# Kernel optimization log

Measured on AMD Instinct MI355X. Metric: run time of the kernel, lower is better.

## Reference

```python
import jax, jax.numpy as jnp
import numpy as np

MODEL_DIM = 256
PAIR_IMPORTANCE_WEIGHT = 0.5
B, S, D = 4, 4096, MODEL_DIM


def setup_inputs() -> dict:
    key = jax.random.key(0)
    ks = jax.random.split(key, 6)
    return {
        "query": jax.random.normal(ks[0], (B, S, D), dtype=jnp.float32),
        "key": jax.random.normal(ks[1], (B, S, D), dtype=jnp.float32),
        "value": jax.random.normal(ks[2], (B, S, D), dtype=jnp.float32),
        "W_query": jax.random.normal(ks[3], (D, D), dtype=jnp.float32),
        "W_key": jax.random.normal(ks[4], (D, D), dtype=jnp.float32),
        "W_value": jax.random.normal(ks[5], (D, D), dtype=jnp.float32),
    }


def reference(query, key, value, W_query, W_key, W_value):
    # Projections: [B,S,D] @ [D,D]
    q = jnp.einsum('bsd,de->bse', query, W_query)
    k = jnp.einsum('bsd,de->bse', key, W_key)
    v = jnp.einsum('bsd,de->bse', value, W_value)
    scale = jnp.sqrt(jnp.asarray(MODEL_DIM, dtype=q.dtype))
    # Full [B,S,S] score matrix (global max forces materialization)
    scores = jnp.einsum('bqd,bkd->bqk', q, k) / scale
    s_len = scores.shape[1]
    diag_bias = jnp.eye(s_len, dtype=scores.dtype) * jnp.max(scores)
    scores = scores + PAIR_IMPORTANCE_WEIGHT * diag_bias  # broadcast over batch
    attention_weights = jax.nn.softmax(scores, axis=-1)
    output = jnp.einsum('bqk,bkd->bqd', attention_weights, v)
    return output, attention_weights
```

## Files before the change

kernel.cpp:

```cpp
#include <hip/hip_runtime.h>
#include <cstdint>
#include <cstddef>

#define BB 4
#define SS 4096
#define DD 256
#define SCORE_SCALE (1.0f/16.0f)
#define PIW 0.5f

typedef float          f32x4  __attribute__((ext_vector_type(4)));
typedef __bf16         bf16v8 __attribute__((ext_vector_type(8)));
typedef unsigned short u16v8  __attribute__((ext_vector_type(8)));
typedef unsigned short u16v4  __attribute__((ext_vector_type(4)));

__device__ __forceinline__ f32x4 mfma_bf16(u16v8 a, u16v8 b, f32x4 c) {
    return __builtin_amdgcn_mfma_f32_16x16x32_bf16(
        __builtin_bit_cast(bf16v8, a), __builtin_bit_cast(bf16v8, b), c, 0, 0, 0);
}

__device__ __forceinline__ unsigned short f2bf(float f) {
    unsigned u = __float_as_uint(f);
    u += 0x7FFFu + ((u >> 16) & 1u);
    return (unsigned short)(u >> 16);
}
__device__ __forceinline__ float bf2f(unsigned short h) {
    return __uint_as_float(((unsigned)h) << 16);
}
__device__ __forceinline__ unsigned fenc(float x) {
    unsigned u = __float_as_uint(x);
    return (u & 0x80000000u) ? ~u : (u | 0x80000000u);
}
__device__ __forceinline__ float fdec(unsigned e) {
    return __uint_as_float((e & 0x80000000u) ? (e ^ 0x80000000u) : ~e);
}

#define TM 128
#define TN 128
#define TK 16
#define PADW 132

__global__ __launch_bounds__(256) void proj_kernel(
    const float* __restrict__ query, const float* __restrict__ key_, const float* __restrict__ value,
    const float* __restrict__ Wq, const float* __restrict__ Wk, const float* __restrict__ Wv,
    unsigned short* __restrict__ qh, unsigned short* __restrict__ ql,
    unsigned short* __restrict__ kh, unsigned short* __restrict__ kl,
    unsigned short* __restrict__ vT, unsigned* __restrict__ gmax)
{
    const int z = blockIdx.z;
    const float* A = (z == 0) ? query : (z == 1) ? key_ : value;
    const float* W = (z == 0) ? Wq    : (z == 1) ? Wk   : Wv;
    if (z == 0 && blockIdx.x == 0 && blockIdx.y == 0 && threadIdx.x == 0)
        *gmax = 0x007FFFFFu;

    const int K = DD, N = DD;
    __shared__ float As[TK][PADW];
    __shared__ float Bs[TK][PADW];
    const int tid = threadIdx.x;
    const int tx = tid & 15, ty = tid >> 4;
    const int rowBase = blockIdx.y * TM;
    const int colBase = blockIdx.x * TN;

    float acc[8][8] = {};

    for (int k0 = 0; k0 < K; k0 += TK) {
        #pragma unroll
        for (int i = 0; i < 2; i++) {
            int idx = tid + i * 256;
            int r = idx >> 2, kq = idx & 3;
            const float4 av = *(const float4*)&A[(size_t)(rowBase + r) * K + k0 + kq * 4];
            As[kq * 4 + 0][r] = av.x; As[kq * 4 + 1][r] = av.y;
            As[kq * 4 + 2][r] = av.z; As[kq * 4 + 3][r] = av.w;
        }
        #pragma unroll
        for (int i = 0; i < 2; i++) {
            int idx = tid + i * 256;
            int kk = idx >> 5, cq = idx & 31;
            *(float4*)&Bs[kk][cq * 4] = *(const float4*)&W[(size_t)(k0 + kk) * N + colBase + cq * 4];
        }
        __syncthreads();
        #pragma unroll
        for (int kk = 0; kk < TK; kk++) {
            float a[8], b[8];
            *(float4*)&a[0] = *(const float4*)&As[kk][ty * 8];
            *(float4*)&a[4] = *(const float4*)&As[kk][ty * 8 + 4];
            *(float4*)&b[0] = *(const float4*)&Bs[kk][tx * 8];
            *(float4*)&b[4] = *(const float4*)&Bs[kk][tx * 8 + 4];
            #pragma unroll
            for (int i = 0; i < 8; i++)
                #pragma unroll
                for (int j = 0; j < 8; j++)
                    acc[i][j] = fmaf(a[i], b[j], acc[i][j]);
        }
        __syncthreads();
    }

    #pragma unroll
    for (int i = 0; i < 8; i++) {
        const int gr = rowBase + ty * 8 + i;
        if (z == 2) {
            const int b2 = gr >> 12, s2 = gr & (SS - 1);
            #pragma unroll
            for (int j = 0; j < 8; j++) {
                int col = colBase + tx * 8 + j;
                vT[((size_t)b2 * DD + col) * SS + s2] = f2bf(acc[i][j]);
            }
        } else {
            unsigned short h[8], l[8];
            #pragma unroll
            for (int j = 0; j < 8; j++) {
                h[j] = f2bf(acc[i][j]);
                l[j] = f2bf(acc[i][j] - bf2f(h[j]));
            }
            unsigned short* H = (z == 0) ? qh : kh;
            unsigned short* L = (z == 0) ? ql : kl;
            size_t base = (size_t)gr * DD + colBase + tx * 8;
            *(u16v4*)&H[base]     = (u16v4){h[0], h[1], h[2], h[3]};
            *(u16v4*)&H[base + 4] = (u16v4){h[4], h[5], h[6], h[7]};
            *(u16v4*)&L[base]     = (u16v4){l[0], l[1], l[2], l[3]};
            *(u16v4*)&L[base + 4] = (u16v4){l[4], l[5], l[6], l[7]};
        }
    }
}

#define SPAD 40

__global__ __launch_bounds__(256) void scores_mfma(
    const unsigned short* __restrict__ qh, const unsigned short* __restrict__ ql,
    const unsigned short* __restrict__ kh, const unsigned short* __restrict__ kl,
    float* __restrict__ attn, unsigned* __restrict__ gmax)
{
    const int b = blockIdx.z;
    const size_t boff = (size_t)b * SS * DD;
    const unsigned short* Qh = qh + boff;
    const unsigned short* Ql = ql + boff;
    const unsigned short* Kh = kh + boff;
    const unsigned short* Kl = kl + boff;
    float* C = attn + (size_t)b * SS * SS;

    __shared__ unsigned short Ah[128][SPAD];
    __shared__ unsigned short Al[128][SPAD];
    __shared__ unsigned short Bh[128][SPAD];
    __shared__ unsigned short Bl[128][SPAD];
    __shared__ float red[256];

    const int tid = threadIdx.x;
    const int lane = tid & 63, w = tid >> 6;
    const int wr = (w >> 1) * 64, wc = (w & 1) * 64;
    const int m = lane & 15, qq = lane >> 4;
    const int rowBase = blockIdx.y * 128;
    const int colBase = blockIdx.x * 128;

    f32x4 acc[4][4];
    #pragma unroll
    for (int i = 0; i < 4; i++)
        #pragma unroll
        for (int j = 0; j < 4; j++)
            acc[i][j] = (f32x4){0.f, 0.f, 0.f, 0.f};

    const int chunk = (tid & 3) * 8;
    const int srow  = tid >> 2;

    for (int k0 = 0; k0 < DD; k0 += 32) {
        #pragma unroll
        for (int i = 0; i < 2; i++) {
            int r = srow + i * 64;
            size_t ga = (size_t)(rowBase + r) * DD + k0 + chunk;
            size_t gb = (size_t)(colBase + r) * DD + k0 + chunk;
            *(u16v8*)&Ah[r][chunk] = *(const u16v8*)&Qh[ga];
            *(u16v8*)&Al[r][chunk] = *(const u16v8*)&Ql[ga];
            *(u16v8*)&Bh[r][chunk] = *(const u16v8*)&Kh[gb];
            *(u16v8*)&Bl[r][chunk] = *(const u16v8*)&Kl[gb];
        }
        __syncthreads();

        const int kb = qq * 8;
        u16v8 ah[4], al[4], bh[4], bl[4];
        #pragma unroll
        for (int i = 0; i < 4; i++) {
            ah[i] = *(const u16v8*)&Ah[wr + i * 16 + m][kb];
            al[i] = *(const u16v8*)&Al[wr + i * 16 + m][kb];
            bh[i] = *(const u16v8*)&Bh[wc + i * 16 + m][kb];
            bl[i] = *(const u16v8*)&Bl[wc + i * 16 + m][kb];
        }
        #pragma unroll
        for (int i = 0; i < 4; i++)
            #pragma unroll
            for (int j = 0; j < 4; j++) {
                acc[i][j] = mfma_bf16(ah[i], bh[j], acc[i][j]);
                acc[i][j] = mfma_bf16(ah[i], bl[j], acc[i][j]);
                acc[i][j] = mfma_bf16(al[i], bh[j], acc[i][j]);
            }
        __syncthreads();
    }

    float mx = -INFINITY;
    #pragma unroll
    for (int i = 0; i < 4; i++) {
        #pragma unroll
        for (int j = 0; j < 4; j++) {
            #pragma unroll
            for (int r = 0; r < 4; r++) {
                float v = acc[i][j][r] * SCORE_SCALE;
                int row = rowBase + wr + i * 16 + qq * 4 + r;
                int col = colBase + wc + j * 16 + m;
                C[(size_t)row * SS + col] = v;
                mx = fmaxf(mx, v);
            }
        }
    }
    red[tid] = mx;
    __syncthreads();
    for (int s2 = 128; s2 > 0; s2 >>= 1) {
        if (tid < s2) red[tid] = fmaxf(red[tid], red[tid + s2]);
        __syncthreads();
    }
    if (tid == 0) atomicMax(gmax, fenc(red[0]));
}

__global__ __launch_bounds__(256) void softmax_kernel(
    float* __restrict__ attn, const unsigned* __restrict__ gmax)
{
    const int row = blockIdx.x;
    const int i = row & (SS - 1);
    float* p = attn + (size_t)row * SS;
    const float bias = PIW * fdec(*gmax);
    const int tid = threadIdx.x;

    float x[16];
    float m = -INFINITY;
    #pragma unroll
    for (int u = 0; u < 4; u++) {
        int j4 = u * 1024 + tid * 4;
        float4 t = *(const float4*)&p[j4];
        float e0 = t.x + ((j4 + 0 == i) ? bias : 0.0f);
        float e1 = t.y + ((j4 + 1 == i) ? bias : 0.0f);
        float e2 = t.z + ((j4 + 2 == i) ? bias : 0.0f);
        float e3 = t.w + ((j4 + 3 == i) ? bias : 0.0f);
        x[u * 4 + 0] = e0; x[u * 4 + 1] = e1; x[u * 4 + 2] = e2; x[u * 4 + 3] = e3;
        m = fmaxf(fmaxf(fmaxf(m, e0), fmaxf(e1, e2)), e3);
    }
    __shared__ float red[256];
    red[tid] = m;
    __syncthreads();
    for (int s2 = 128; s2 > 0; s2 >>= 1) {
        if (tid < s2) red[tid] = fmaxf(red[tid], red[tid + s2]);
        __syncthreads();
    }
    const float rm = red[0];
    __syncthreads();

    float s = 0.0f;
    #pragma unroll
    for (int u = 0; u < 16; u++) {
        x[u] = __expf(x[u] - rm);
        s += x[u];
    }
    red[tid] = s;
    __syncthreads();
    for (int s2 = 128; s2 > 0; s2 >>= 1) {
        if (tid < s2) red[tid] += red[tid + s2];
        __syncthreads();
    }
    const float inv = 1.0f / red[0];
    #pragma unroll
    for (int u = 0; u < 4; u++) {
        int j4 = u * 1024 + tid * 4;
        float4 o = make_float4(x[u*4+0] * inv, x[u*4+1] * inv, x[u*4+2] * inv, x[u*4+3] * inv);
        *(float4*)&p[j4] = o;
    }
}

#define APAD 72

__global__ __launch_bounds__(256) void av_mfma(
    const float* __restrict__ attn, const unsigned short* __restrict__ vT,
    float* __restrict__ out)
{
    const int b = blockIdx.y;
    const int rowBase = blockIdx.x * 32;
    const float* A = attn + (size_t)b * SS * SS;
    const unsigned short* Bv = vT + (size_t)b * DD * SS;

    __shared__ unsigned short As[32][APAD];
    __shared__ unsigned short Bs[256][APAD];

    const int tid = threadIdx.x;
    const int lane = tid & 63, w = tid >> 6;
    const int m = lane & 15, qq = lane >> 4;

    f32x4 acc[2][4];
    #pragma unroll
    for (int i = 0; i < 2; i++)
        #pragma unroll
        for (int j = 0; j < 4; j++)
            acc[i][j] = (f32x4){0.f, 0.f, 0.f, 0.f};

    for (int k0 = 0; k0 < SS; k0 += 64) {
        {
            const int ch = tid & 15;
            #pragma unroll
            for (int i = 0; i < 2; i++) {
                int r = (tid >> 4) + i * 16;
                float4 t = *(const float4*)&A[(size_t)(rowBase + r) * SS + k0 + ch * 4];
                u16v4 s = (u16v4){f2bf(t.x), f2bf(t.y), f2bf(t.z), f2bf(t.w)};
                *(u16v4*)&As[r][ch * 4] = s;
            }
        }
        {
            const int ch = (tid & 7) * 8;
            #pragma unroll
            for (int i = 0; i < 8; i++) {
                int r = (tid >> 3) + i * 32;
                *(u16v8*)&Bs[r][ch] = *(const u16v8*)&Bv[(size_t)r * SS + k0 + ch];
            }
        }
        __syncthreads();

        #pragma unroll
        for (int kk = 0; kk < 64; kk += 32) {
            const int kb = kk + qq * 8;
            u16v8 af[2], bf[4];
            #pragma unroll
            for (int i = 0; i < 2; i++)
                af[i] = *(const u16v8*)&As[i * 16 + m][kb];
            #pragma unroll
            for (int j = 0; j < 4; j++)
                bf[j] = *(const u16v8*)&Bs[w * 64 + j * 16 + m][kb];
            #pragma unroll
            for (int i = 0; i < 2; i++)
                #pragma unroll
                for (int j = 0; j < 4; j++)
                    acc[i][j] = mfma_bf16(af[i], bf[j], acc[i][j]);
        }
        __syncthreads();
    }

    #pragma unroll
    for (int i = 0; i < 2; i++) {
        #pragma unroll
        for (int j = 0; j < 4; j++) {
            #pragma unroll
            for (int r = 0; r < 4; r++) {
                int row = rowBase + i * 16 + qq * 4 + r;
                int col = w * 64 + j * 16 + m;
                out[((size_t)b * SS + row) * DD + col] = acc[i][j][r];
            }
        }
    }
}

extern "C" void kernel_launch(void* const* d_in, const int* in_sizes, int n_in,
                              void* d_out, int out_size, void* d_ws, size_t ws_size,
                              hipStream_t stream)
{
    const float* query = (const float*)d_in[0];
    const float* key_  = (const float*)d_in[1];
    const float* value = (const float*)d_in[2];
    const float* Wq    = (const float*)d_in[3];
    const float* Wk    = (const float*)d_in[4];
    const float* Wv    = (const float*)d_in[5];

    float* out  = (float*)d_out;
    float* attn = out + (size_t)BB * SS * DD;

    const size_t E = (size_t)BB * SS * DD;
    unsigned short* qh = (unsigned short*)d_ws;
    unsigned short* ql = qh + E;
    unsigned short* kh = ql + E;
    unsigned short* kl = kh + E;
    unsigned short* vT = kl + E;
    unsigned* gmax = (unsigned*)(vT + E);

    proj_kernel<<<dim3(DD / TN, (BB * SS) / TM, 3), 256, 0, stream>>>(
        query, key_, value, Wq, Wk, Wv, qh, ql, kh, kl, vT, gmax);
    scores_mfma<<<dim3(SS / 128, SS / 128, BB), 256, 0, stream>>>(
        qh, ql, kh, kl, attn, gmax);
    softmax_kernel<<<dim3(BB * SS), 256, 0, stream>>>(attn, gmax);
    av_mfma<<<dim3(SS / 32, BB), 256, 0, stream>>>(attn, vT, out);
}
```

Before: 684.1 us.

## Fuse softmax into AV kernel using per-tile online row statistics from scores kernel

The scores kernel now computes per-tile row max and exp-sum and writes them to workspace. A small merge kernel combines these into per-row max and inverse sum, correcting for the diagonal bias. The AV kernel then applies exp and normalisation on the fly, writes the final weights back and feeds them into the MFMA. This removes the standalone softmax pass and its extra full read and write of the 4096x4096 score matrix, at the cost of more epilogue work in the scores kernel and exp work inside the AV inner loop.

```diff
diff --git a/kernel.cpp b/kernel.cpp
--- a/kernel.cpp
+++ b/kernel.cpp
@@ -7,6 +7,7 @@
 #define DD 256
 #define SCORE_SCALE (1.0f/16.0f)
 #define PIW 0.5f
+#define NROWS (BB * SS)
 
 typedef float          f32x4  __attribute__((ext_vector_type(4)));
 typedef __bf16         bf16v8 __attribute__((ext_vector_type(8)));
@@ -127,7 +128,8 @@
 __global__ __launch_bounds__(256) void scores_mfma(
     const unsigned short* __restrict__ qh, const unsigned short* __restrict__ ql,
     const unsigned short* __restrict__ kh, const unsigned short* __restrict__ kl,
-    float* __restrict__ attn, unsigned* __restrict__ gmax)
+    float* __restrict__ attn, unsigned* __restrict__ gmax,
+    float* __restrict__ tmaxg, float* __restrict__ tsumg)
 {
     const int b = blockIdx.z;
     const size_t boff = (size_t)b * SS * DD;
@@ -141,7 +143,9 @@
     __shared__ unsigned short Al[128][SPAD];
     __shared__ unsigned short Bh[128][SPAD];
     __shared__ unsigned short Bl[128][SPAD];
-    __shared__ float red[256];
+    __shared__ float s_m[4][64];
+    __shared__ float s_s[4][64];
+    __shared__ float red[128];
 
     const int tid = threadIdx.x;
     const int lane = tid & 63, w = tid >> 6;
@@ -193,93 +197,130 @@
         __syncthreads();
     }
 
-    float mx = -INFINITY;
-    #pragma unroll
-    for (int i = 0; i < 4; i++) {
-        #pragma unroll
-        for (int j = 0; j < 4; j++) {
+    #pragma unroll
+    for (int i = 0; i < 4; i++)
+        #pragma unroll
+        for (int j = 0; j < 4; j++)
+            acc[i][j] *= SCORE_SCALE;
+
+    #pragma unroll
+    for (int i = 0; i < 4; i++)
+        #pragma unroll
+        for (int j = 0; j < 4; j++)
             #pragma unroll
             for (int r = 0; r < 4; r++) {
-                float v = acc[i][j][r] * SCORE_SCALE;
                 int row = rowBase + wr + i * 16 + qq * 4 + r;
                 int col = colBase + wc + j * 16 + m;
-                C[(size_t)row * SS + col] = v;
-                mx = fmaxf(mx, v);
-            }
-        }
-    }
-    red[tid] = mx;
+                C[(size_t)row * SS + col] = acc[i][j][r];
+            }
+
+    float lmax[16];
+    #pragma unroll
+    for (int i = 0; i < 4; i++)
+        #pragma unroll
+        for (int r = 0; r < 4; r++)
+            lmax[i * 4 + r] = fmaxf(fmaxf(acc[i][0][r], acc[i][1][r]),
+                                    fmaxf(acc[i][2][r], acc[i][3][r]));
+    #pragma unroll
+    for (int t = 0; t < 16; t++) {
+        #pragma unroll
+        for (int msk = 1; msk < 16; msk <<= 1)
+            lmax[t] = fmaxf(lmax[t], __shfl_xor(lmax[t], msk));
+    }
+    if (m == 0) {
+        #pragma unroll
+        for (int i = 0; i < 4; i++)
+            #pragma unroll
+            for (int r = 0; r < 4; r++)
+                s_m[w][i * 16 + qq * 4 + r] = lmax[i * 4 + r];
+    }
     __syncthreads();
-    for (int s2 = 128; s2 > 0; s2 >>= 1) {
+    float lsum[16];
+    #pragma unroll
+    for (int i = 0; i < 4; i++)
+        #pragma unroll
+        for (int r = 0; r < 4; r++) {
+            int idx = i * 16 + qq * 4 + r;
+            float rm = fmaxf(s_m[w][idx], s_m[w ^ 1][idx]);
+            float s = 0.f;
+            #pragma unroll
+            for (int j = 0; j < 4; j++)
+                s += __expf(acc[i][j][r] - rm);
+            lsum[i * 4 + r] = s;
+        }
+    #pragma unroll
+    for (int t = 0; t < 16; t++) {
+        #pragma unroll
+        for (int msk = 1; msk < 16; msk <<= 1)
+            lsum[t] += __shfl_xor(lsum[t], msk);
+    }
+    if (m == 0) {
+        #pragma unroll
+        for (int i = 0; i < 4; i++)
+            #pragma unroll
+            for (int r = 0; r < 4; r++)
+                s_s[w][i * 16 + qq * 4 + r] = lsum[i * 4 + r];
+    }
+    __syncthreads();
+
+    if (tid < 128) {
+        int wp = tid >> 6, lr = tid & 63;
+        float tm = fmaxf(s_m[2 * wp][lr], s_m[2 * wp + 1][lr]);
+        float ts = s_s[2 * wp][lr] + s_s[2 * wp + 1][lr];
+        size_t gi = (size_t)blockIdx.x * NROWS + (size_t)b * SS + rowBase + tid;
+        tmaxg[gi] = tm;
+        tsumg[gi] = ts;
+        red[tid] = tm;
+    }
+    __syncthreads();
+    for (int s2 = 64; s2 > 0; s2 >>= 1) {
         if (tid < s2) red[tid] = fmaxf(red[tid], red[tid + s2]);
         __syncthreads();
     }
     if (tid == 0) atomicMax(gmax, fenc(red[0]));
 }
 
-__global__ __launch_bounds__(256) void softmax_kernel(
-    float* __restrict__ attn, const unsigned* __restrict__ gmax)
+__global__ __launch_bounds__(256) void stats_merge(
+    const float* __restrict__ tmaxg, const float* __restrict__ tsumg,
+    const float* __restrict__ attn, const unsigned* __restrict__ gmax,
+    float* __restrict__ rowm, float* __restrict__ rowinv)
 {
-    const int row = blockIdx.x;
-    const int i = row & (SS - 1);
-    float* p = attn + (size_t)row * SS;
+    const int grow = blockIdx.x * 256 + threadIdx.x;
+    const int b = grow >> 12, i = grow & (SS - 1);
     const float bias = PIW * fdec(*gmax);
-    const int tid = threadIdx.x;
-
-    float x[16];
-    float m = -INFINITY;
-    #pragma unroll
-    for (int u = 0; u < 4; u++) {
-        int j4 = u * 1024 + tid * 4;
-        float4 t = *(const float4*)&p[j4];
-        float e0 = t.x + ((j4 + 0 == i) ? bias : 0.0f);
-        float e1 = t.y + ((j4 + 1 == i) ? bias : 0.0f);
-        float e2 = t.z + ((j4 + 2 == i) ? bias : 0.0f);
-        float e3 = t.w + ((j4 + 3 == i) ? bias : 0.0f);
-        x[u * 4 + 0] = e0; x[u * 4 + 1] = e1; x[u * 4 + 2] = e2; x[u * 4 + 3] = e3;
-        m = fmaxf(fmaxf(fmaxf(m, e0), fmaxf(e1, e2)), e3);
-    }
-    __shared__ float red[256];
-    red[tid] = m;
-    __syncthreads();
-    for (int s2 = 128; s2 > 0; s2 >>= 1) {
-        if (tid < s2) red[tid] = fmaxf(red[tid], red[tid + s2]);
-        __syncthreads();
-    }
-    const float rm = red[0];
-    __syncthreads();
-
-    float s = 0.0f;
-    #pragma unroll
-    for (int u = 0; u < 16; u++) {
-        x[u] = __expf(x[u] - rm);
-        s += x[u];
-    }
-    red[tid] = s;
-    __syncthreads();
-    for (int s2 = 128; s2 > 0; s2 >>= 1) {
-        if (tid < s2) red[tid] += red[tid + s2];
-        __syncthreads();
-    }
-    const float inv = 1.0f / red[0];
-    #pragma unroll
-    for (int u = 0; u < 4; u++) {
-        int j4 = u * 1024 + tid * 4;
-        float4 o = make_float4(x[u*4+0] * inv, x[u*4+1] * inv, x[u*4+2] * inv, x[u*4+3] * inv);
-        *(float4*)&p[j4] = o;
-    }
+
+    float tm[32];
+    float mx = -INFINITY;
+    #pragma unroll
+    for (int t = 0; t < 32; t++) {
+        tm[t] = tmaxg[(size_t)t * NROWS + grow];
+        mx = fmaxf(mx, tm[t]);
+    }
+    const float dii = attn[(size_t)b * SS * SS + (size_t)i * SS + i];
+    mx = fmaxf(mx, dii + bias);
+
+    float s = 0.f;
+    #pragma unroll
+    for (int t = 0; t < 32; t++)
+        s += tsumg[(size_t)t * NROWS + grow] * __expf(tm[t] - mx);
+    s += __expf(dii + bias - mx) - __expf(dii - mx);
+
+    rowm[grow] = mx;
+    rowinv[grow] = 1.0f / s;
 }
 
 #define APAD 72
 
-__global__ __launch_bounds__(256) void av_mfma(
-    const float* __restrict__ attn, const unsigned short* __restrict__ vT,
-    float* __restrict__ out)
+__global__ __launch_bounds__(256) void av_softmax_mfma(
+    float* __restrict__ attn, const unsigned short* __restrict__ vT,
+    const float* __restrict__ rowm, const float* __restrict__ rowinv,
+    const unsigned* __restrict__ gmax, float* __restrict__ out)
 {
     const int b = blockIdx.y;
     const int rowBase = blockIdx.x * 32;
-    const float* A = attn + (size_t)b * SS * SS;
+    float* A = attn + (size_t)b * SS * SS;
     const unsigned short* Bv = vT + (size_t)b * DD * SS;
+    const float bias = PIW * fdec(*gmax);
 
     __shared__ unsigned short As[32][APAD];
     __shared__ unsigned short Bs[256][APAD];
@@ -288,6 +329,16 @@
     const int lane = tid & 63, w = tid >> 6;
     const int m = lane & 15, qq = lane >> 4;
 
+    const int ch = tid & 15;
+    const int ra = tid >> 4;
+    float mr[2], ri[2];
+    #pragma unroll
+    for (int i = 0; i < 2; i++) {
+        int rr = rowBase + ra + i * 16;
+        mr[i] = rowm[b * SS + rr];
+        ri[i] = rowinv[b * SS + rr];
+    }
+
     f32x4 acc[2][4];
     #pragma unroll
     for (int i = 0; i < 2; i++)
@@ -296,22 +347,30 @@
             acc[i][j] = (f32x4){0.f, 0.f, 0.f, 0.f};
 
     for (int k0 = 0; k0 < SS; k0 += 64) {
+        #pragma unroll
+        for (int i = 0; i < 2; i++) {
+            int rr = rowBase + ra + i * 16;
+            size_t off = (size_t)rr * SS + k0 + ch * 4;
+            float4 t = *(const float4*)&A[off];
+            int j0 = k0 + ch * 4;
+            float e0 = t.x + ((j0 + 0 == rr) ? bias : 0.0f);
+            float e1 = t.y + ((j0 + 1 == rr) ? bias : 0.0f);
+            float e2 = t.z + ((j0 + 2 == rr) ? bias : 0.0f);
+            float e3 = t.w + ((j0 + 3 == rr) ? bias : 0.0f);
+            float w0 = __expf(e0 - mr[i]) * ri[i];
+            float w1 = __expf(e1 - mr[i]) * ri[i];
+            float w2 = __expf(e2 - mr[i]) * ri[i];
+            float w3 = __expf(e3 - mr[i]) * ri[i];
+            *(float4*)&A[off] = make_float4(w0, w1, w2, w3);
+            *(u16v4*)&As[ra + i * 16][ch * 4] =
+                (u16v4){f2bf(w0), f2bf(w1), f2bf(w2), f2bf(w3)};
+        }
         {
-            const int ch = tid & 15;
-            #pragma unroll
-            for (int i = 0; i < 2; i++) {
-                int r = (tid >> 4) + i * 16;
-                float4 t = *(const float4*)&A[(size_t)(rowBase + r) * SS + k0 + ch * 4];
-                u16v4 s = (u16v4){f2bf(t.x), f2bf(t.y), f2bf(t.z), f2bf(t.w)};
-                *(u16v4*)&As[r][ch * 4] = s;
-            }
-        }
-        {
-            const int ch = (tid & 7) * 8;
+            const int chb = (tid & 7) * 8;
             #pragma unroll
             for (int i = 0; i < 8; i++) {
                 int r = (tid >> 3) + i * 32;
-                *(u16v8*)&Bs[r][ch] = *(const u16v8*)&Bv[(size_t)r * SS + k0 + ch];
+                *(u16v8*)&Bs[r][chb] = *(const u16v8*)&Bv[(size_t)r * SS + k0 + chb];
             }
         }
         __syncthreads();
@@ -369,12 +428,18 @@
     unsigned short* kh = ql + E;
     unsigned short* kl = kh + E;
     unsigned short* vT = kl + E;
-    unsigned* gmax = (unsigned*)(vT + E);
+    float* tmaxg  = (float*)(vT + E);
+    float* tsumg  = tmaxg + 32 * (size_t)NROWS;
+    float* rowm   = tsumg + 32 * (size_t)NROWS;
+    float* rowinv = rowm + NROWS;
+    unsigned* gmax = (unsigned*)(rowinv + NROWS);
 
     proj_kernel<<<dim3(DD / TN, (BB * SS) / TM, 3), 256, 0, stream>>>(
         query, key_, value, Wq, Wk, Wv, qh, ql, kh, kl, vT, gmax);
     scores_mfma<<<dim3(SS / 128, SS / 128, BB), 256, 0, stream>>>(
-        qh, ql, kh, kl, attn, gmax);
-    softmax_kernel<<<dim3(BB * SS), 256, 0, stream>>>(attn, gmax);
-    av_mfma<<<dim3(SS / 32, BB), 256, 0, stream>>>(attn, vT, out);
-}
+        qh, ql, kh, kl, attn, gmax, tmaxg, tsumg);
+    stats_merge<<<dim3(NROWS / 256), 256, 0, stream>>>(
+        tmaxg, tsumg, attn, gmax, rowm, rowinv);
+    av_softmax_mfma<<<dim3(SS / 32, BB), 256, 0, stream>>>(
+        attn, vT, rowm, rowinv, gmax, out);
+}
```

New measurement: 729.5 us. 6.6% more time.
